# Performance work log

Measured on AMD Instinct MI355X. Metric: run time of the kernel, lower is better.

## Reference

```python
import jax, jax.numpy as jnp
import numpy as np

B, D, C = 16384, 2048, 1000  # batch, in_features (feature dim), out_features (classes)
INIT_SCALE = 10.0
EPS = 1e-12


def setup_inputs() -> dict:
    key = jax.random.key(0)
    k1, k2 = jax.random.split(key)
    x = jax.random.normal(k1, (B, D), dtype=jnp.float32)
    weights = jax.random.normal(k2, (C, D), dtype=jnp.float32)  # prototypes
    scales = jnp.ones((1,), dtype=jnp.float32) * INIT_SCALE
    return {"x": x, "weights": weights, "scales": scales}


def reference(x, weights, scales):
    # Pairwise Euclidean distance between features [B,D] and prototypes [C,D]
    x2 = jnp.sum(x * x, axis=-1, keepdims=True)            # [B,1]
    w2 = jnp.sum(weights * weights, axis=-1)               # [C]
    cross = jnp.einsum('bd,cd->bc', x, weights)            # [B,C]
    d2 = jnp.maximum(x2 + w2[None, :] - 2.0 * cross, EPS)  # clamp for sqrt stability
    distances = jnp.sqrt(d2)                               # [B,C]
    logits = -scales * distances  # dml forward: -self.learn(distances)
    return logits
```

## Files before the change

kernel.cpp:

```cpp
#include <hip/hip_runtime.h>
#include <hip/hip_bf16.h>
#include <stdint.h>

#define B_ROWS 16384
#define D_K    2048
#define C_COLS 1000
#define C_PAD  1024
#define EPS_D2 1e-12f

#define BM 256
#define BN 256
#define BK 32
#define NT (D_K / BK)
#define BUF_BYTES 32768
#define NBUF 4

typedef __attribute__((ext_vector_type(8))) short bf16x8;
typedef __attribute__((ext_vector_type(4))) float f32x4;

__device__ __forceinline__ void async16(void* lds, const void* g) {
    __builtin_amdgcn_global_load_lds(
        (const __attribute__((address_space(1))) unsigned int*)g,
        (__attribute__((address_space(3))) unsigned int*)lds,
        16, 0, 0);
}

__device__ __forceinline__ uint2 pack_bf16x4(float4 v) {
    union { __hip_bfloat162 h; uint32_t u; } a, b;
    a.h = __float22bfloat162_rn(make_float2(v.x, v.y));
    b.h = __float22bfloat162_rn(make_float2(v.z, v.w));
    uint2 r; r.x = a.u; r.y = b.u; return r;
}

__global__ __launch_bounds__(256) void prep_all(
    const float* __restrict__ x, const float* __restrict__ w,
    __hip_bfloat16* __restrict__ xb, __hip_bfloat16* __restrict__ wb,
    float* __restrict__ x2, float* __restrict__ w2) {
    const int t = threadIdx.x;
    const int wave = t >> 6;
    const int lane = t & 63;
    const int row = blockIdx.x * 4 + wave;

    const float* src;
    uint4* dst;
    float* norm_out;
    bool valid;
    if (row < B_ROWS) {
        src = x + (size_t)row * D_K;
        dst = (uint4*)(xb + (size_t)row * D_K);
        norm_out = x2 + row;
        valid = true;
    } else {
        int c = row - B_ROWS;
        src = w + (size_t)c * D_K;
        dst = (uint4*)(wb + (size_t)c * D_K);
        norm_out = w2 + c;
        valid = (c < C_COLS);
    }

    float4 v[8];
    if (valid) {
        const float4* s4 = (const float4*)src;
        #pragma unroll
        for (int i = 0; i < 4; i++) {
            v[2 * i]     = s4[2 * lane + 128 * i];
            v[2 * i + 1] = s4[2 * lane + 1 + 128 * i];
        }
    } else {
        #pragma unroll
        for (int i = 0; i < 8; i++) v[i] = make_float4(0.f, 0.f, 0.f, 0.f);
    }

    float ss = 0.f;
    #pragma unroll
    for (int i = 0; i < 8; i++)
        ss += v[i].x * v[i].x + v[i].y * v[i].y + v[i].z * v[i].z + v[i].w * v[i].w;

    #pragma unroll
    for (int i = 0; i < 4; i++) {
        uint2 a = pack_bf16x4(v[2 * i]);
        uint2 b = pack_bf16x4(v[2 * i + 1]);
        uint4 p; p.x = a.x; p.y = a.y; p.z = b.x; p.w = b.y;
        dst[lane + 64 * i] = p;
    }

    #pragma unroll
    for (int off = 32; off > 0; off >>= 1) ss += __shfl_down(ss, off, 64);
    if (lane == 0 && valid) *norm_out = ss;
}

__global__ __launch_bounds__(512, 2) void dml_gemm(
    const __hip_bfloat16* __restrict__ A,
    const __hip_bfloat16* __restrict__ Bm,
    const float* __restrict__ x2, const float* __restrict__ w2,
    const float* __restrict__ scales, float* __restrict__ out)
{
    __shared__ __align__(16) char smem[NBUF * BUF_BYTES];

    const int tid  = threadIdx.x;
    const int wave = tid >> 6;
    const int lane = tid & 63;
    const int wm = wave >> 2;
    const int wn = wave & 3;

    const int id  = blockIdx.x;
    const int xcd = id & 7;
    const int j5  = id >> 3;
    const int m0  = (xcd * 8 + (j5 & 7)) * BM;
    const int n0  = (j5 >> 3) * BN;

    const int L0 = tid, L1 = tid + 512;
    const int r0 = L0 >> 2, g0 = (L0 & 3) ^ ((r0 >> 1) & 3);
    const int r1 = L1 >> 2, g1 = (L1 & 3) ^ ((r1 >> 1) & 3);
    const __hip_bfloat16* pA0 = A  + (size_t)(m0 + r0) * D_K + g0 * 8;
    const __hip_bfloat16* pA1 = A  + (size_t)(m0 + r1) * D_K + g1 * 8;
    const __hip_bfloat16* pB0 = Bm + (size_t)(n0 + r0) * D_K + g0 * 8;
    const __hip_bfloat16* pB1 = Bm + (size_t)(n0 + r1) * D_K + g1 * 8;
    char* ldA0 = smem + L0 * 16;
    char* ldA1 = smem + L1 * 16;
    char* ldB0 = smem + 16384 + L0 * 16;
    char* ldB1 = smem + 16384 + L1 * 16;

    const int fr = lane & 15;
    const int fq = lane >> 4;
    const int ksw = (fq ^ ((fr >> 1) & 3)) * 16;
    const char* fA = smem + (wm * 128 + fr) * 64 + ksw;
    const char* fB = smem + 16384 + (wn * 64 + fr) * 64 + ksw;

    f32x4 acc[8][4] = {};

    #pragma unroll
    for (int tgt = 0; tgt < 3; ++tgt) {
        const int sbo = tgt * BUF_BYTES;
        async16(ldA0 + sbo, pA0 + tgt * BK);
        async16(ldA1 + sbo, pA1 + tgt * BK);
        async16(ldB0 + sbo, pB0 + tgt * BK);
        async16(ldB1 + sbo, pB1 + tgt * BK);
    }
    asm volatile("s_waitcnt vmcnt(8)" ::: "memory");
    __builtin_amdgcn_s_barrier();
    __builtin_amdgcn_sched_barrier(0);

    #pragma unroll 1
    for (int t = 0; t < NT; ++t) {
        const int bo  = (t & 3) * BUF_BYTES;
        const int tgt = t + 3;
        const bool do_stage = (tgt < NT);
        const int sbo = (tgt & 3) * BUF_BYTES;

        if (do_stage) {
            async16(ldA0 + sbo, pA0 + tgt * BK);
            async16(ldA1 + sbo, pA1 + tgt * BK);
        }
        bf16x8 b[4], a[4];
        #pragma unroll
        for (int q = 0; q < 4; ++q) b[q] = *(const bf16x8*)(fB + bo + q * 1024);
        #pragma unroll
        for (int i = 0; i < 4; ++i) a[i] = *(const bf16x8*)(fA + bo + i * 1024);
        __builtin_amdgcn_s_setprio(1);
        #pragma unroll
        for (int i = 0; i < 4; ++i)
            #pragma unroll
            for (int q = 0; q < 4; ++q)
                acc[i][q] = __builtin_amdgcn_mfma_f32_16x16x32_bf16(a[i], b[q], acc[i][q], 0, 0, 0);
        __builtin_amdgcn_s_setprio(0);

        if (do_stage) {
            async16(ldB0 + sbo, pB0 + tgt * BK);
            async16(ldB1 + sbo, pB1 + tgt * BK);
        }
        #pragma unroll
        for (int i = 0; i < 4; ++i) a[i] = *(const bf16x8*)(fA + bo + (4 + i) * 1024);
        __builtin_amdgcn_s_setprio(1);
        #pragma unroll
        for (int i = 0; i < 4; ++i)
            #pragma unroll
            for (int q = 0; q < 4; ++q)
                acc[4 + i][q] = __builtin_amdgcn_mfma_f32_16x16x32_bf16(a[i], b[q], acc[4 + i][q], 0, 0, 0);
        __builtin_amdgcn_s_setprio(0);

        if (t < NT - 3)      asm volatile("s_waitcnt vmcnt(8)" ::: "memory");
        else if (t == NT - 3) asm volatile("s_waitcnt vmcnt(4)" ::: "memory");
        else if (t == NT - 2) asm volatile("s_waitcnt vmcnt(0)" ::: "memory");
        if (t < NT - 1) {
            __builtin_amdgcn_s_barrier();
            __builtin_amdgcn_sched_barrier(0);
        }
    }

    const float s = scales[0];
    const int colb = n0 + wn * 64 + fr;
    const int rowb = m0 + wm * 128 + fq * 4;

    float w2v[4];
    #pragma unroll
    for (int q = 0; q < 4; ++q) w2v[q] = w2[colb + q * 16];

    #pragma unroll
    for (int i = 0; i < 8; ++i) {
        float x2v[4];
        #pragma unroll
        for (int r = 0; r < 4; ++r) x2v[r] = x2[rowb + i * 16 + r];
        #pragma unroll
        for (int q = 0; q < 4; ++q) {
            if (colb + q * 16 < C_COLS) {
                float* orow = out + (size_t)(rowb + i * 16) * C_COLS + colb + q * 16;
                #pragma unroll
                for (int r = 0; r < 4; ++r) {
                    float d2 = x2v[r] + w2v[q] - 2.0f * acc[i][q][r];
                    d2 = fmaxf(d2, EPS_D2);
                    orow[(size_t)r * C_COLS] = -s * __builtin_sqrtf(d2);
                }
            }
        }
    }
}

extern "C" void kernel_launch(void* const* d_in, const int* in_sizes, int n_in,
                              void* d_out, int out_size, void* d_ws, size_t ws_size,
                              hipStream_t stream) {
    const float* x      = (const float*)d_in[0];
    const float* w      = (const float*)d_in[1];
    const float* scales = (const float*)d_in[2];
    float* out = (float*)d_out;

    char* ws = (char*)d_ws;
    __hip_bfloat16* xb = (__hip_bfloat16*)ws;
    __hip_bfloat16* wb = (__hip_bfloat16*)(ws + (size_t)B_ROWS * D_K * 2);
    float* x2 = (float*)(ws + (size_t)B_ROWS * D_K * 2 + (size_t)C_PAD * D_K * 2);
    float* w2 = x2 + B_ROWS;

    prep_all<<<dim3((B_ROWS + C_PAD) / 4), dim3(256), 0, stream>>>(x, w, xb, wb, x2, w2);
    dml_gemm<<<dim3((B_ROWS / BM) * (C_PAD / BN)), dim3(512), 0, stream>>>(xb, wb, x2, w2, scales, out);
}
```

Baseline: 286.7 us.

## Fuse x bf16 conversion and row norms into the GEMM A-tile loader

Removes the separate pass that converted x to bf16 and computed its squared norms. The GEMM now loads fp32 x into registers, packs it to bf16, and writes it into double-buffered LDS, accumulating the row norms along the way. Those norms are reduced at the end and read from shared memory in the epilogue. The W side keeps its async global-to-LDS pipeline with four buffers. This drops the 64MB bf16 intermediate and a full read of x, but the GEMM now reads fp32 x across four N-blocks and stages A through registers, which adds latency and register pressure.

```diff
diff --git a/kernel.cpp b/kernel.cpp
--- a/kernel.cpp
+++ b/kernel.cpp
@@ -12,8 +12,6 @@
 #define BN 256
 #define BK 32
 #define NT (D_K / BK)
-#define BUF_BYTES 32768
-#define NBUF 4
 
 typedef __attribute__((ext_vector_type(8))) short bf16x8;
 typedef __attribute__((ext_vector_type(4))) float f32x4;
@@ -32,31 +30,21 @@
     uint2 r; r.x = a.u; r.y = b.u; return r;
 }
 
-__global__ __launch_bounds__(256) void prep_all(
-    const float* __restrict__ x, const float* __restrict__ w,
-    __hip_bfloat16* __restrict__ xb, __hip_bfloat16* __restrict__ wb,
-    float* __restrict__ x2, float* __restrict__ w2) {
+__device__ __forceinline__ float sq4(float4 v) {
+    return v.x * v.x + v.y * v.y + v.z * v.z + v.w * v.w;
+}
+
+__global__ __launch_bounds__(256) void prep_w(
+    const float* __restrict__ w, __hip_bfloat16* __restrict__ wb,
+    float* __restrict__ w2) {
     const int t = threadIdx.x;
     const int wave = t >> 6;
     const int lane = t & 63;
-    const int row = blockIdx.x * 4 + wave;
-
-    const float* src;
-    uint4* dst;
-    float* norm_out;
-    bool valid;
-    if (row < B_ROWS) {
-        src = x + (size_t)row * D_K;
-        dst = (uint4*)(xb + (size_t)row * D_K);
-        norm_out = x2 + row;
-        valid = true;
-    } else {
-        int c = row - B_ROWS;
-        src = w + (size_t)c * D_K;
-        dst = (uint4*)(wb + (size_t)c * D_K);
-        norm_out = w2 + c;
-        valid = (c < C_COLS);
-    }
+    const int c = blockIdx.x * 4 + wave;
+    const bool valid = (c < C_COLS);
+
+    const float* src = w + (size_t)c * D_K;
+    uint4* dst = (uint4*)(wb + (size_t)c * D_K);
 
     float4 v[8];
     if (valid) {
@@ -73,8 +61,7 @@
 
     float ss = 0.f;
     #pragma unroll
-    for (int i = 0; i < 8; i++)
-        ss += v[i].x * v[i].x + v[i].y * v[i].y + v[i].z * v[i].z + v[i].w * v[i].w;
+    for (int i = 0; i < 8; i++) ss += sq4(v[i]);
 
     #pragma unroll
     for (int i = 0; i < 4; i++) {
@@ -86,16 +73,16 @@
 
     #pragma unroll
     for (int off = 32; off > 0; off >>= 1) ss += __shfl_down(ss, off, 64);
-    if (lane == 0 && valid) *norm_out = ss;
+    if (lane == 0 && valid) w2[c] = ss;
 }
 
 __global__ __launch_bounds__(512, 2) void dml_gemm(
-    const __hip_bfloat16* __restrict__ A,
+    const float* __restrict__ X,
     const __hip_bfloat16* __restrict__ Bm,
-    const float* __restrict__ x2, const float* __restrict__ w2,
+    const float* __restrict__ w2,
     const float* __restrict__ scales, float* __restrict__ out)
 {
-    __shared__ __align__(16) char smem[NBUF * BUF_BYTES];
+    __shared__ __align__(16) char smem[98304];
 
     const int tid  = threadIdx.x;
     const int wave = tid >> 6;
@@ -112,51 +99,80 @@
     const int L0 = tid, L1 = tid + 512;
     const int r0 = L0 >> 2, g0 = (L0 & 3) ^ ((r0 >> 1) & 3);
     const int r1 = L1 >> 2, g1 = (L1 & 3) ^ ((r1 >> 1) & 3);
-    const __hip_bfloat16* pA0 = A  + (size_t)(m0 + r0) * D_K + g0 * 8;
-    const __hip_bfloat16* pA1 = A  + (size_t)(m0 + r1) * D_K + g1 * 8;
-    const __hip_bfloat16* pB0 = Bm + (size_t)(n0 + r0) * D_K + g0 * 8;
-    const __hip_bfloat16* pB1 = Bm + (size_t)(n0 + r1) * D_K + g1 * 8;
-    char* ldA0 = smem + L0 * 16;
-    char* ldA1 = smem + L1 * 16;
-    char* ldB0 = smem + 16384 + L0 * 16;
-    char* ldB1 = smem + 16384 + L1 * 16;
-
-    const int fr = lane & 15;
-    const int fq = lane >> 4;
-    const int ksw = (fq ^ ((fr >> 1) & 3)) * 16;
-    const char* fA = smem + (wm * 128 + fr) * 64 + ksw;
-    const char* fB = smem + 16384 + (wn * 64 + fr) * 64 + ksw;
+    const float* gAf0 = X + (size_t)(m0 + r0) * D_K + g0 * 8;
+    const float* gAf1 = X + (size_t)(m0 + r1) * D_K + g1 * 8;
+    const __hip_bfloat16* gB0 = Bm + (size_t)(n0 + r0) * D_K + g0 * 8;
+    const __hip_bfloat16* gB1 = Bm + (size_t)(n0 + r1) * D_K + g1 * 8;
+    char* ldB0 = smem + 32768 + L0 * 16;
+    char* ldB1 = smem + 32768 + L1 * 16;
+
+    const int fr  = lane & 15;
+    const int fq  = lane >> 4;
+    const int fsw = (fr >> 1) & 3;
+    const char* fA = smem + (wm * 128 + fr) * 64 + (fq ^ fsw) * 16;
+    const char* fB = smem + 32768 + (wn * 64 + fr) * 64 + (fq ^ fsw) * 16;
 
     f32x4 acc[8][4] = {};
-
-    #pragma unroll
-    for (int tgt = 0; tgt < 3; ++tgt) {
-        const int sbo = tgt * BUF_BYTES;
-        async16(ldA0 + sbo, pA0 + tgt * BK);
-        async16(ldA1 + sbo, pA1 + tgt * BK);
-        async16(ldB0 + sbo, pB0 + tgt * BK);
-        async16(ldB1 + sbo, pB1 + tgt * BK);
-    }
-    asm volatile("s_waitcnt vmcnt(8)" ::: "memory");
+    float s0 = 0.f, s1 = 0.f;
+
+    float4 va0, va1, va2, va3;
+    {
+        const float4* q0 = (const float4*)(gAf0);
+        const float4* q1 = (const float4*)(gAf1);
+        va0 = q0[0]; va1 = q0[1]; va2 = q1[0]; va3 = q1[1];
+        const float4* p0 = (const float4*)(gAf0 + 32);
+        const float4* p1 = (const float4*)(gAf1 + 32);
+        float4 vb0 = p0[0], vb1 = p0[1], vb2 = p1[0], vb3 = p1[1];
+        async16(ldB0 + 0,     gB0);        async16(ldB1 + 0,     gB1);
+        async16(ldB0 + 16384, gB0 + 32);   async16(ldB1 + 16384, gB1 + 32);
+        async16(ldB0 + 32768, gB0 + 64);   async16(ldB1 + 32768, gB1 + 64);
+        uint2 c0 = pack_bf16x4(va0), c1 = pack_bf16x4(va1);
+        uint2 c2 = pack_bf16x4(va2), c3 = pack_bf16x4(va3);
+        uint4 p; p.x = c0.x; p.y = c0.y; p.z = c1.x; p.w = c1.y;
+        *(uint4*)(smem + L0 * 16) = p;
+        p.x = c2.x; p.y = c2.y; p.z = c3.x; p.w = c3.y;
+        *(uint4*)(smem + L1 * 16) = p;
+        s0 += sq4(va0) + sq4(va1);
+        s1 += sq4(va2) + sq4(va3);
+        va0 = vb0; va1 = vb1; va2 = vb2; va3 = vb3;
+    }
+    asm volatile("s_waitcnt vmcnt(4)" ::: "memory");
+    asm volatile("s_waitcnt lgkmcnt(0)" ::: "memory");
     __builtin_amdgcn_s_barrier();
     __builtin_amdgcn_sched_barrier(0);
 
     #pragma unroll 1
     for (int t = 0; t < NT; ++t) {
-        const int bo  = (t & 3) * BUF_BYTES;
-        const int tgt = t + 3;
-        const bool do_stage = (tgt < NT);
-        const int sbo = (tgt & 3) * BUF_BYTES;
-
-        if (do_stage) {
-            async16(ldA0 + sbo, pA0 + tgt * BK);
-            async16(ldA1 + sbo, pA1 + tgt * BK);
-        }
+        const int boA = (t & 1) * 16384;
+        const int boB = (t & 3) * 16384;
+
+        if (t < NT - 1) {
+            char* dA = smem + ((t + 1) & 1) * 16384;
+            uint2 c0 = pack_bf16x4(va0), c1 = pack_bf16x4(va1);
+            uint2 c2 = pack_bf16x4(va2), c3 = pack_bf16x4(va3);
+            uint4 p; p.x = c0.x; p.y = c0.y; p.z = c1.x; p.w = c1.y;
+            *(uint4*)(dA + L0 * 16) = p;
+            p.x = c2.x; p.y = c2.y; p.z = c3.x; p.w = c3.y;
+            *(uint4*)(dA + L1 * 16) = p;
+            s0 += sq4(va0) + sq4(va1);
+            s1 += sq4(va2) + sq4(va3);
+            if (t + 2 < NT) {
+                const float4* q0 = (const float4*)(gAf0 + (t + 2) * 32);
+                const float4* q1 = (const float4*)(gAf1 + (t + 2) * 32);
+                va0 = q0[0]; va1 = q0[1]; va2 = q1[0]; va3 = q1[1];
+            }
+        }
+        if (t + 3 < NT) {
+            const int sbo = ((t + 3) & 3) * 16384;
+            async16(ldB0 + sbo, gB0 + (t + 3) * BK);
+            async16(ldB1 + sbo, gB1 + (t + 3) * BK);
+        }
+
         bf16x8 b[4], a[4];
         #pragma unroll
-        for (int q = 0; q < 4; ++q) b[q] = *(const bf16x8*)(fB + bo + q * 1024);
-        #pragma unroll
-        for (int i = 0; i < 4; ++i) a[i] = *(const bf16x8*)(fA + bo + i * 1024);
+        for (int q = 0; q < 4; ++q) b[q] = *(const bf16x8*)(fB + boB + q * 1024);
+        #pragma unroll
+        for (int i = 0; i < 4; ++i) a[i] = *(const bf16x8*)(fA + boA + i * 1024);
         __builtin_amdgcn_s_setprio(1);
         #pragma unroll
         for (int i = 0; i < 4; ++i)
@@ -164,13 +180,8 @@
             for (int q = 0; q < 4; ++q)
                 acc[i][q] = __builtin_amdgcn_mfma_f32_16x16x32_bf16(a[i], b[q], acc[i][q], 0, 0, 0);
         __builtin_amdgcn_s_setprio(0);
-
-        if (do_stage) {
-            async16(ldB0 + sbo, pB0 + tgt * BK);
-            async16(ldB1 + sbo, pB1 + tgt * BK);
-        }
-        #pragma unroll
-        for (int i = 0; i < 4; ++i) a[i] = *(const bf16x8*)(fA + bo + (4 + i) * 1024);
+        #pragma unroll
+        for (int i = 0; i < 4; ++i) a[i] = *(const bf16x8*)(fA + boA + (4 + i) * 1024);
         __builtin_amdgcn_s_setprio(1);
         #pragma unroll
         for (int i = 0; i < 4; ++i)
@@ -179,14 +190,24 @@
                 acc[4 + i][q] = __builtin_amdgcn_mfma_f32_16x16x32_bf16(a[i], b[q], acc[4 + i][q], 0, 0, 0);
         __builtin_amdgcn_s_setprio(0);
 
-        if (t < NT - 3)      asm volatile("s_waitcnt vmcnt(8)" ::: "memory");
+        if (t < NT - 3)       asm volatile("s_waitcnt vmcnt(6)" ::: "memory");
         else if (t == NT - 3) asm volatile("s_waitcnt vmcnt(4)" ::: "memory");
-        else if (t == NT - 2) asm volatile("s_waitcnt vmcnt(0)" ::: "memory");
         if (t < NT - 1) {
+            asm volatile("s_waitcnt lgkmcnt(0)" ::: "memory");
             __builtin_amdgcn_s_barrier();
             __builtin_amdgcn_sched_barrier(0);
         }
     }
+
+    __syncthreads();
+    s0 += __shfl_xor(s0, 1, 64); s0 += __shfl_xor(s0, 2, 64);
+    s1 += __shfl_xor(s1, 1, 64); s1 += __shfl_xor(s1, 2, 64);
+    float* smx = (float*)smem;
+    if ((lane & 3) == 0) {
+        smx[r0] = s0;
+        smx[r0 + 128] = s1;
+    }
+    __syncthreads();
 
     const float s = scales[0];
     const int colb = n0 + wn * 64 + fr;
@@ -200,7 +221,8 @@
     for (int i = 0; i < 8; ++i) {
         float x2v[4];
         #pragma unroll
-        for (int r = 0; r < 4; ++r) x2v[r] = x2[rowb + i * 16 + r];
+        for (int r = 0; r < 4; ++r)
+            x2v[r] = smx[wm * 128 + i * 16 + fq * 4 + r];
         #pragma unroll
         for (int q = 0; q < 4; ++q) {
             if (colb + q * 16 < C_COLS) {
@@ -225,11 +247,9 @@
     float* out = (float*)d_out;
 
     char* ws = (char*)d_ws;
-    __hip_bfloat16* xb = (__hip_bfloat16*)ws;
-    __hip_bfloat16* wb = (__hip_bfloat16*)(ws + (size_t)B_ROWS * D_K * 2);
-    float* x2 = (float*)(ws + (size_t)B_ROWS * D_K * 2 + (size_t)C_PAD * D_K * 2);
-    float* w2 = x2 + B_ROWS;
-
-    prep_all<<<dim3((B_ROWS + C_PAD) / 4), dim3(256), 0, stream>>>(x, w, xb, wb, x2, w2);
-    dml_gemm<<<dim3((B_ROWS / BM) * (C_PAD / BN)), dim3(512), 0, stream>>>(xb, wb, x2, w2, scales, out);
-}
+    __hip_bfloat16* wb = (__hip_bfloat16*)ws;
+    float* w2 = (float*)(ws + (size_t)C_PAD * D_K * 2);
+
+    prep_w<<<dim3(C_PAD / 4), dim3(256), 0, stream>>>(w, wb, w2);
+    dml_gemm<<<dim3((B_ROWS / BM) * (C_PAD / BN)), dim3(512), 0, stream>>>(x, wb, w2, scales, out);
+}
```

Measured after the change: 294.3 us. 2.7% more time.

## Shrink GEMM tile to 256x128 with triple buffering and higher occupancy

Applied to the files above, without the earlier changes.

The output tile width is halved to 128, and the 8 waves are rearranged into a 4x2 grid, so each wave computes a 64x64 sub-tile. The LDS pipeline drops from four to three stages of 24 KB, and the launch-bounds occupancy hint rises from 2 to 4 blocks. This doubles the block count to 512, which can give the GPU more blocks per CU to schedule and hide latency. In exchange, each block does less MFMA work per LDS fragment load, the A matrix is streamed from memory twice as often, and the pipeline is one stage shallower.

```diff
diff --git a/kernel.cpp b/kernel.cpp
--- a/kernel.cpp
+++ b/kernel.cpp
@@ -9,11 +9,11 @@
 #define EPS_D2 1e-12f
 
 #define BM 256
-#define BN 256
+#define BN 128
 #define BK 32
 #define NT (D_K / BK)
-#define BUF_BYTES 32768
-#define NBUF 4
+#define BUFB 24576
+#define NBUF 3
 
 typedef __attribute__((ext_vector_type(8))) short bf16x8;
 typedef __attribute__((ext_vector_type(4))) float f32x4;
@@ -89,19 +89,19 @@
     if (lane == 0 && valid) *norm_out = ss;
 }
 
-__global__ __launch_bounds__(512, 2) void dml_gemm(
+__global__ __launch_bounds__(512, 4) void dml_gemm(
     const __hip_bfloat16* __restrict__ A,
     const __hip_bfloat16* __restrict__ Bm,
     const float* __restrict__ x2, const float* __restrict__ w2,
     const float* __restrict__ scales, float* __restrict__ out)
 {
-    __shared__ __align__(16) char smem[NBUF * BUF_BYTES];
+    __shared__ __align__(16) char smem[NBUF * BUFB];
 
     const int tid  = threadIdx.x;
     const int wave = tid >> 6;
     const int lane = tid & 63;
-    const int wm = wave >> 2;
-    const int wn = wave & 3;
+    const int wm = wave >> 1;
+    const int wn = wave & 1;
 
     const int id  = blockIdx.x;
     const int xcd = id & 7;
@@ -112,46 +112,37 @@
     const int L0 = tid, L1 = tid + 512;
     const int r0 = L0 >> 2, g0 = (L0 & 3) ^ ((r0 >> 1) & 3);
     const int r1 = L1 >> 2, g1 = (L1 & 3) ^ ((r1 >> 1) & 3);
+    const int rB = tid >> 2, gB = (tid & 3) ^ ((rB >> 1) & 3);
     const __hip_bfloat16* pA0 = A  + (size_t)(m0 + r0) * D_K + g0 * 8;
     const __hip_bfloat16* pA1 = A  + (size_t)(m0 + r1) * D_K + g1 * 8;
-    const __hip_bfloat16* pB0 = Bm + (size_t)(n0 + r0) * D_K + g0 * 8;
-    const __hip_bfloat16* pB1 = Bm + (size_t)(n0 + r1) * D_K + g1 * 8;
+    const __hip_bfloat16* pB  = Bm + (size_t)(n0 + rB) * D_K + gB * 8;
     char* ldA0 = smem + L0 * 16;
     char* ldA1 = smem + L1 * 16;
-    char* ldB0 = smem + 16384 + L0 * 16;
-    char* ldB1 = smem + 16384 + L1 * 16;
-
-    const int fr = lane & 15;
-    const int fq = lane >> 4;
-    const int ksw = (fq ^ ((fr >> 1) & 3)) * 16;
-    const char* fA = smem + (wm * 128 + fr) * 64 + ksw;
-    const char* fB = smem + 16384 + (wn * 64 + fr) * 64 + ksw;
-
-    f32x4 acc[8][4] = {};
-
-    #pragma unroll
-    for (int tgt = 0; tgt < 3; ++tgt) {
-        const int sbo = tgt * BUF_BYTES;
-        async16(ldA0 + sbo, pA0 + tgt * BK);
-        async16(ldA1 + sbo, pA1 + tgt * BK);
-        async16(ldB0 + sbo, pB0 + tgt * BK);
-        async16(ldB1 + sbo, pB1 + tgt * BK);
-    }
-    asm volatile("s_waitcnt vmcnt(8)" ::: "memory");
+    char* ldB  = smem + 16384 + tid * 16;
+
+    const int fr  = lane & 15;
+    const int fq  = lane >> 4;
+    const int fsw = (fr >> 1) & 3;
+    const char* fA = smem + (wm * 64 + fr) * 64 + (fq ^ fsw) * 16;
+    const char* fB = smem + 16384 + (wn * 64 + fr) * 64 + (fq ^ fsw) * 16;
+
+    f32x4 acc[4][4] = {};
+
+    async16(ldA0,        pA0);      async16(ldA1,        pA1);      async16(ldB,        pB);
+    async16(ldA0 + BUFB, pA0 + 32); async16(ldA1 + BUFB, pA1 + 32); async16(ldB + BUFB, pB + 32);
+    asm volatile("s_waitcnt vmcnt(3)" ::: "memory");
     __builtin_amdgcn_s_barrier();
     __builtin_amdgcn_sched_barrier(0);
 
+    int bo = 0, sbo = 2 * BUFB;
     #pragma unroll 1
     for (int t = 0; t < NT; ++t) {
-        const int bo  = (t & 3) * BUF_BYTES;
-        const int tgt = t + 3;
-        const bool do_stage = (tgt < NT);
-        const int sbo = (tgt & 3) * BUF_BYTES;
-
-        if (do_stage) {
-            async16(ldA0 + sbo, pA0 + tgt * BK);
-            async16(ldA1 + sbo, pA1 + tgt * BK);
-        }
+        if (t + 2 < NT) {
+            async16(ldA0 + sbo, pA0 + (t + 2) * BK);
+            async16(ldA1 + sbo, pA1 + (t + 2) * BK);
+            async16(ldB  + sbo, pB  + (t + 2) * BK);
+        }
+
         bf16x8 b[4], a[4];
         #pragma unroll
         for (int q = 0; q < 4; ++q) b[q] = *(const bf16x8*)(fB + bo + q * 1024);
@@ -165,39 +156,26 @@
                 acc[i][q] = __builtin_amdgcn_mfma_f32_16x16x32_bf16(a[i], b[q], acc[i][q], 0, 0, 0);
         __builtin_amdgcn_s_setprio(0);
 
-        if (do_stage) {
-            async16(ldB0 + sbo, pB0 + tgt * BK);
-            async16(ldB1 + sbo, pB1 + tgt * BK);
-        }
-        #pragma unroll
-        for (int i = 0; i < 4; ++i) a[i] = *(const bf16x8*)(fA + bo + (4 + i) * 1024);
-        __builtin_amdgcn_s_setprio(1);
-        #pragma unroll
-        for (int i = 0; i < 4; ++i)
-            #pragma unroll
-            for (int q = 0; q < 4; ++q)
-                acc[4 + i][q] = __builtin_amdgcn_mfma_f32_16x16x32_bf16(a[i], b[q], acc[4 + i][q], 0, 0, 0);
-        __builtin_amdgcn_s_setprio(0);
-
-        if (t < NT - 3)      asm volatile("s_waitcnt vmcnt(8)" ::: "memory");
-        else if (t == NT - 3) asm volatile("s_waitcnt vmcnt(4)" ::: "memory");
+        if (t < NT - 2)       asm volatile("s_waitcnt vmcnt(3)" ::: "memory");
         else if (t == NT - 2) asm volatile("s_waitcnt vmcnt(0)" ::: "memory");
         if (t < NT - 1) {
             __builtin_amdgcn_s_barrier();
             __builtin_amdgcn_sched_barrier(0);
         }
+        bo  = (bo  == 2 * BUFB) ? 0 : bo  + BUFB;
+        sbo = (sbo == 2 * BUFB) ? 0 : sbo + BUFB;
     }
 
     const float s = scales[0];
     const int colb = n0 + wn * 64 + fr;
-    const int rowb = m0 + wm * 128 + fq * 4;
+    const int rowb = m0 + wm * 64 + fq * 4;
 
     float w2v[4];
     #pragma unroll
     for (int q = 0; q < 4; ++q) w2v[q] = w2[colb + q * 16];
 
     #pragma unroll
-    for (int i = 0; i < 8; ++i) {
+    for (int i = 0; i < 4; ++i) {
         float x2v[4];
         #pragma unroll
         for (int r = 0; r < 4; ++r) x2v[r] = x2[rowb + i * 16 + r];
```

New measurement: 297.9 us. 3.9% more time.
